# Kernel tuning notes

Measured on AMD Instinct MI355X. Metric: run time of the kernel, lower is better.

Reference implementation:

```python
import jax, jax.numpy as jnp
import numpy as np

B, S, H, NH, L, NS = 8, 4096, 768, 12, 2, 64
DH = H // NH
EPS = 1e-12


def _layer_norm(x, g, b):
    mu = jnp.mean(x, axis=-1, keepdims=True)
    var = jnp.mean((x - mu) ** 2, axis=-1, keepdims=True)
    return (x - mu) / jnp.sqrt(var + EPS) * g + b


def setup_inputs() -> dict:
    key = jax.random.key(0)
    ks = jax.random.split(key, 8)
    # sentence index per token: 64 equal contiguous sentences; position 0 is [CLS] in sentence 0
    sent_ind = jnp.broadcast_to((jnp.arange(S, dtype=jnp.int32) * NS) // S, (B, S)).astype(jnp.int32)
    start_layer = jax.random.normal(ks[0], (B, S, H), dtype=jnp.float32)
    init = lambda k, shape: (jax.random.normal(k, shape, dtype=jnp.float32) * 0.02)
    return {
        "sent_ind": sent_ind,
        "start_layer": start_layer,
        "Wq": init(ks[1], (L, H, H)), "bq": jnp.zeros((L, H), jnp.float32),
        "Wk": init(ks[2], (L, H, H)), "bk": jnp.zeros((L, H), jnp.float32),
        "Wv": init(ks[3], (L, H, H)), "bv": jnp.zeros((L, H), jnp.float32),
        "Wo": init(ks[4], (L, H, H)), "bo": jnp.zeros((L, H), jnp.float32),
        "ln_g": jnp.ones((L, H), jnp.float32), "ln_b": jnp.zeros((L, H), jnp.float32),
    }


def reference(sent_ind, start_layer, Wq, bq, Wk, bk, Wv, bv, Wo, bo, ln_g, ln_b):
    # ---- segment-mean pooling by sentence index (vectorized replacement of the python loops) ----
    onehot = (sent_ind[..., None] == jnp.arange(NS, dtype=sent_ind.dtype)).astype(start_layer.dtype)  # [B,S,NS]
    # the first [CLS] token is excluded from sentence 0's mean
    onehot = onehot.at[:, 0, :].set(0.0)
    sums = jnp.einsum('bsn,bsd->bnd', onehot, start_layer)          # [B,NS,H]
    counts = jnp.sum(onehot, axis=1)                                 # [B,NS]
    x = sums / counts[..., None]                                     # graph_vectors [B,NS,H]

    # ---- GAT layers: BertSelfAttention + GATSelfOutput(dense->gelu->LayerNorm), dropout=eval ----
    scale = 1.0 / (DH ** 0.5)
    for i in range(L):
        q = (x @ Wq[i] + bq[i]).reshape(B, NS, NH, DH)
        k = (x @ Wk[i] + bk[i]).reshape(B, NS, NH, DH)
        v = (x @ Wv[i] + bv[i]).reshape(B, NS, NH, DH)
        scores = jnp.einsum('bqhd,bkhd->bhqk', q, k) * scale
        probs = jax.nn.softmax(scores, axis=-1)
        ctx = jnp.einsum('bhqk,bkhd->bqhd', probs, v).reshape(B, NS, H)
        h = jax.nn.gelu(ctx @ Wo[i] + bo[i], approximate=False)
        x = _layer_norm(h, ln_g[i], ln_b[i])
    return x
```

## Files before the change

### kernel.cpp

```cpp
#include <hip/hip_runtime.h>
#include <hip/hip_bf16.h>

constexpr int cB  = 8;
constexpr int cS  = 4096;
constexpr int cH  = 768;
constexpr int cNH = 12;
constexpr int cL  = 2;
constexpr int cNS = 64;
constexpr int cDH = 64;
constexpr int cM  = cB * cNS;

typedef __attribute__((ext_vector_type(8))) short bf16x8;
typedef __attribute__((ext_vector_type(4))) float f32x4;

union PrepShared {
    float T[64][65];
    struct { int cnt; int list[cS]; } p;
};

__global__ __launch_bounds__(256) void prep_kernel(
    const int* __restrict__ sent_ind, const float* __restrict__ sl,
    __hip_bfloat16* __restrict__ xb,
    const float* __restrict__ Wq, const float* __restrict__ Wk,
    const float* __restrict__ Wv, const float* __restrict__ Wo,
    __hip_bfloat16* __restrict__ wt)
{
    __shared__ PrepShared sh;
    int tid = threadIdx.x;

    if (blockIdx.x < (unsigned)cM) {
        int bn = blockIdx.x;
        int b = bn >> 6, n = bn & (cNS - 1);
        if (tid == 0) sh.p.cnt = 0;
        __syncthreads();
        const int* si = sent_ind + (size_t)b * cS;
        for (int s = tid; s < cS; s += 256)
            if (s != 0 && si[s] == n) { int p = atomicAdd(&sh.p.cnt, 1); sh.p.list[p] = s; }
        __syncthreads();
        int c = sh.p.cnt;
        if (tid < 192) {
            const float* bbase = sl + (size_t)b * cS * cH;
            int col = tid * 4;
            float4 a0 = {0.f, 0.f, 0.f, 0.f};
            float4 a1 = {0.f, 0.f, 0.f, 0.f};
            float4 a2 = {0.f, 0.f, 0.f, 0.f};
            float4 a3 = {0.f, 0.f, 0.f, 0.f};
            int i = 0;
            for (; i + 4 <= c; i += 4) {
                float4 r0 = *(const float4*)(bbase + (size_t)sh.p.list[i + 0] * cH + col);
                float4 r1 = *(const float4*)(bbase + (size_t)sh.p.list[i + 1] * cH + col);
                float4 r2 = *(const float4*)(bbase + (size_t)sh.p.list[i + 2] * cH + col);
                float4 r3 = *(const float4*)(bbase + (size_t)sh.p.list[i + 3] * cH + col);
                a0.x += r0.x; a0.y += r0.y; a0.z += r0.z; a0.w += r0.w;
                a1.x += r1.x; a1.y += r1.y; a1.z += r1.z; a1.w += r1.w;
                a2.x += r2.x; a2.y += r2.y; a2.z += r2.z; a2.w += r2.w;
                a3.x += r3.x; a3.y += r3.y; a3.z += r3.z; a3.w += r3.w;
            }
            for (; i < c; ++i) {
                float4 r0 = *(const float4*)(bbase + (size_t)sh.p.list[i] * cH + col);
                a0.x += r0.x; a0.y += r0.y; a0.z += r0.z; a0.w += r0.w;
            }
            float inv = 1.0f / (float)c;
            __hip_bfloat16* xr = xb + (size_t)bn * cH + col;
            xr[0] = __float2bfloat16((a0.x + a1.x + a2.x + a3.x) * inv);
            xr[1] = __float2bfloat16((a0.y + a1.y + a2.y + a3.y) * inv);
            xr[2] = __float2bfloat16((a0.z + a1.z + a2.z + a3.z) * inv);
            xr[3] = __float2bfloat16((a0.w + a1.w + a2.w + a3.w) * inv);
        }
    } else {
        int bi = blockIdx.x - cM;
        int bx = bi % 12, by = (bi / 12) % 12, mat = bi / 144;
        int layer = mat >> 2, which = mat & 3;
        const float* W = (which == 0 ? Wq : which == 1 ? Wk : which == 2 ? Wv : Wo)
                         + (size_t)layer * cH * cH;
        int k0 = by * 64, n0 = bx * 64;
        int r = tid >> 2, cb = (tid & 3) * 16;
        #pragma unroll
        for (int u = 0; u < 4; ++u) {
            float4 w4 = *(const float4*)(W + (size_t)(k0 + r) * cH + n0 + cb + u * 4);
            sh.T[r][cb + u * 4 + 0] = w4.x; sh.T[r][cb + u * 4 + 1] = w4.y;
            sh.T[r][cb + u * 4 + 2] = w4.z; sh.T[r][cb + u * 4 + 3] = w4.w;
        }
        __syncthreads();
        int kk = tid & 63;
        int nb = (tid >> 6) * 16;
        __hip_bfloat16* dst = wt + ((size_t)mat * cH + n0) * cH + k0;
        #pragma unroll
        for (int u = 0; u < 16; ++u) {
            int nn = nb + u;
            dst[(size_t)nn * cH + kk] = __float2bfloat16(sh.T[kk][nn]);
        }
    }
}

struct AttnShared {
    float QP[cNS][cDH + 4];
    float Ks[cNS][cDH + 4];
    float Vt[cDH][cNS + 4];
};

__global__ __launch_bounds__(256) void qkvattn_kernel(
    const __hip_bfloat16* __restrict__ x_bf,
    const __hip_bfloat16* __restrict__ wqkv,
    const float* __restrict__ bq, const float* __restrict__ bk,
    const float* __restrict__ bv,
    __hip_bfloat16* __restrict__ ctx_bf)
{
    __shared__ AttnShared sh;
    int tid = threadIdx.x;
    int lane = tid & 63, wave = tid >> 6;
    int l15 = lane & 15, q4 = lane >> 4;
    int b = blockIdx.x / cNH, hh = blockIdx.x % cNH;

    const __hip_bfloat16* Arow[4];
    #pragma unroll
    for (int m = 0; m < 4; ++m)
        Arow[m] = x_bf + (size_t)(b * 64 + m * 16 + l15) * cH + q4 * 8;
    const __hip_bfloat16* Brow[3];
    int cmat[3], cnt_[3];
    #pragma unroll
    for (int j = 0; j < 3; ++j) {
        int c = wave * 3 + j;
        cmat[j] = c >> 2; cnt_[j] = c & 3;
        Brow[j] = wqkv + (size_t)cmat[j] * cH * cH
                       + (size_t)(hh * 64 + cnt_[j] * 16 + l15) * cH + q4 * 8;
    }

    f32x4 acc[3][4];
    #pragma unroll
    for (int j = 0; j < 3; ++j)
        #pragma unroll
        for (int m = 0; m < 4; ++m) acc[j][m] = (f32x4){0.f, 0.f, 0.f, 0.f};

    #pragma unroll 4
    for (int k0 = 0; k0 < cH; k0 += 32) {
        bf16x8 a[4], bb8[3];
        #pragma unroll
        for (int m = 0; m < 4; ++m) a[m] = *(const bf16x8*)(Arow[m] + k0);
        #pragma unroll
        for (int j = 0; j < 3; ++j) bb8[j] = *(const bf16x8*)(Brow[j] + k0);
        #pragma unroll
        for (int j = 0; j < 3; ++j)
            #pragma unroll
            for (int m = 0; m < 4; ++m)
                acc[j][m] = __builtin_amdgcn_mfma_f32_16x16x32_bf16(a[m], bb8[j], acc[j][m], 0, 0, 0);
    }

    const float scale = 0.125f;
    #pragma unroll
    for (int j = 0; j < 3; ++j) {
        int mat = cmat[j], nt = cnt_[j];
        int col_d = nt * 16 + l15;
        int col_g = hh * 64 + col_d;
        float bias = (mat == 0 ? bq : mat == 1 ? bk : bv)[col_g];
        #pragma unroll
        for (int m = 0; m < 4; ++m) {
            #pragma unroll
            for (int r = 0; r < 4; ++r) {
                int row_s = m * 16 + q4 * 4 + r;
                float v = acc[j][m][r] + bias;
                if (mat == 0)      sh.QP[row_s][col_d] = v * scale;
                else if (mat == 1) sh.Ks[row_s][col_d] = v;
                else               sh.Vt[col_d][row_s] = v;
            }
        }
    }
    __syncthreads();

    int tx = tid & 15, ty = tid >> 4;
    float accs[4][4] = {};
    for (int d = 0; d < cDH; d += 4) {
        float4 qv[4], kv[4];
        #pragma unroll
        for (int i = 0; i < 4; ++i) qv[i] = *(const float4*)&sh.QP[ty * 4 + i][d];
        #pragma unroll
        for (int j = 0; j < 4; ++j) kv[j] = *(const float4*)&sh.Ks[tx + j * 16][d];
        #pragma unroll
        for (int i = 0; i < 4; ++i)
            #pragma unroll
            for (int j = 0; j < 4; ++j)
                accs[i][j] += qv[i].x * kv[j].x + qv[i].y * kv[j].y +
                              qv[i].z * kv[j].z + qv[i].w * kv[j].w;
    }
    __syncthreads();
    #pragma unroll
    for (int i = 0; i < 4; ++i)
        #pragma unroll
        for (int j = 0; j < 4; ++j)
            sh.QP[ty * 4 + i][tx + j * 16] = accs[i][j];
    __syncthreads();

    {
        int row = tid >> 2, jq = tid & 3;
        float e[16];
        float m = -1e30f;
        #pragma unroll
        for (int c = 0; c < 16; ++c) { e[c] = sh.QP[row][jq * 16 + c]; m = fmaxf(m, e[c]); }
        m = fmaxf(m, __shfl_xor(m, 1));
        m = fmaxf(m, __shfl_xor(m, 2));
        float s = 0.f;
        #pragma unroll
        for (int c = 0; c < 16; ++c) { e[c] = __expf(e[c] - m); s += e[c]; }
        s += __shfl_xor(s, 1);
        s += __shfl_xor(s, 2);
        float inv = 1.0f / s;
        #pragma unroll
        for (int c = 0; c < 16; ++c) sh.QP[row][jq * 16 + c] = e[c] * inv;
    }
    __syncthreads();

    float acco[4][4] = {};
    for (int c = 0; c < cNS; c += 4) {
        float4 p4[4], vt4[4];
        #pragma unroll
        for (int i = 0; i < 4; ++i) p4[i] = *(const float4*)&sh.QP[ty * 4 + i][c];
        #pragma unroll
        for (int j = 0; j < 4; ++j) vt4[j] = *(const float4*)&sh.Vt[tx + j * 16][c];
        #pragma unroll
        for (int i = 0; i < 4; ++i)
            #pragma unroll
            for (int j = 0; j < 4; ++j)
                acco[i][j] += p4[i].x * vt4[j].x + p4[i].y * vt4[j].y +
                              p4[i].z * vt4[j].z + p4[i].w * vt4[j].w;
    }
    size_t base = ((size_t)b * cNS) * cH + hh * cDH;
    #pragma unroll
    for (int i = 0; i < 4; ++i)
        #pragma unroll
        for (int j = 0; j < 4; ++j)
            ctx_bf[base + (size_t)(ty * 4 + i) * cH + tx + j * 16] =
                __float2bfloat16(acco[i][j]);
}

__global__ __launch_bounds__(256) void oln_kernel(
    const __hip_bfloat16* __restrict__ ctx_bf,
    const __hip_bfloat16* __restrict__ wto,
    const float* __restrict__ bo,
    const float* __restrict__ g, const float* __restrict__ bb,
    __hip_bfloat16* __restrict__ xb, float* __restrict__ outf)
{
    __shared__ float part[4][16][2];
    int tid = threadIdx.x;
    int lane = tid & 63, wave = tid >> 6;
    int l15 = lane & 15, q4 = lane >> 4;
    int r0 = blockIdx.x * 16;

    const __hip_bfloat16* Arow = ctx_bf + (size_t)(r0 + l15) * cH + q4 * 8;
    const __hip_bfloat16* Brow[12];
    #pragma unroll
    for (int nt = 0; nt < 12; ++nt)
        Brow[nt] = wto + (size_t)(wave * 192 + nt * 16 + l15) * cH + q4 * 8;

    f32x4 acc[12];
    #pragma unroll
    for (int nt = 0; nt < 12; ++nt) acc[nt] = (f32x4){0.f, 0.f, 0.f, 0.f};

    #pragma unroll 2
    for (int k0 = 0; k0 < cH; k0 += 32) {
        bf16x8 a = *(const bf16x8*)(Arow + k0);
        #pragma unroll
        for (int nt = 0; nt < 12; ++nt) {
            bf16x8 b8 = *(const bf16x8*)(Brow[nt] + k0);
            acc[nt] = __builtin_amdgcn_mfma_f32_16x16x32_bf16(a, b8, acc[nt], 0, 0, 0);
        }
    }

    float rs[4] = {0.f, 0.f, 0.f, 0.f}, rq[4] = {0.f, 0.f, 0.f, 0.f};
    #pragma unroll
    for (int nt = 0; nt < 12; ++nt) {
        int col = wave * 192 + nt * 16 + l15;
        float bv = bo[col];
        #pragma unroll
        for (int r = 0; r < 4; ++r) {
            float v = acc[nt][r] + bv;
            v = 0.5f * v * (1.0f + erff(v * 0.70710678118654752f));
            acc[nt][r] = v;
            rs[r] += v;
            rq[r] += v * v;
        }
    }
    #pragma unroll
    for (int o = 8; o; o >>= 1) {
        #pragma unroll
        for (int r = 0; r < 4; ++r) {
            rs[r] += __shfl_xor(rs[r], o);
            rq[r] += __shfl_xor(rq[r], o);
        }
    }
    if (l15 == 0) {
        #pragma unroll
        for (int r = 0; r < 4; ++r) {
            part[wave][q4 * 4 + r][0] = rs[r];
            part[wave][q4 * 4 + r][1] = rq[r];
        }
    }
    __syncthreads();
    #pragma unroll
    for (int r = 0; r < 4; ++r) {
        int row = q4 * 4 + r;
        float S  = part[0][row][0] + part[1][row][0] + part[2][row][0] + part[3][row][0];
        float Q2 = part[0][row][1] + part[1][row][1] + part[2][row][1] + part[3][row][1];
        float mu  = S * (1.0f / 768.0f);
        float var = Q2 * (1.0f / 768.0f) - mu * mu;
        float inv = rsqrtf(var + 1e-12f);
        int row_g = r0 + row;
        #pragma unroll
        for (int nt = 0; nt < 12; ++nt) {
            int col = wave * 192 + nt * 16 + l15;
            float o = (acc[nt][r] - mu) * inv * g[col] + bb[col];
            xb[(size_t)row_g * cH + col] = __float2bfloat16(o);
            if (outf) outf[(size_t)row_g * cH + col] = o;
        }
    }
}

extern "C" void kernel_launch(void* const* d_in, const int* in_sizes, int n_in,
                              void* d_out, int out_size, void* d_ws, size_t ws_size,
                              hipStream_t stream) {
    const int*   sent_ind = (const int*)d_in[0];
    const float* start    = (const float*)d_in[1];
    const float* Wq = (const float*)d_in[2];
    const float* bq = (const float*)d_in[3];
    const float* Wk = (const float*)d_in[4];
    const float* bk = (const float*)d_in[5];
    const float* Wv = (const float*)d_in[6];
    const float* bv = (const float*)d_in[7];
    const float* Wo = (const float*)d_in[8];
    const float* bo = (const float*)d_in[9];
    const float* ln_g = (const float*)d_in[10];
    const float* ln_b = (const float*)d_in[11];
    float* out = (float*)d_out;

    char* w = (char*)d_ws;
    __hip_bfloat16* wt     = (__hip_bfloat16*)w;
    __hip_bfloat16* x_bf   = (__hip_bfloat16*)(w + 9437184);
    __hip_bfloat16* ctx_bf = (__hip_bfloat16*)(w + 9437184 + 786432);

    prep_kernel<<<cM + 1152, 256, 0, stream>>>(sent_ind, start, x_bf,
                                               Wq, Wk, Wv, Wo, wt);

    for (int i = 0; i < cL; ++i) {
        const __hip_bfloat16* wqkv = wt + (size_t)(i * 4) * cH * cH;
        const __hip_bfloat16* wto  = wt + (size_t)(i * 4 + 3) * cH * cH;
        qkvattn_kernel<<<cB * cNH, 256, 0, stream>>>(
            x_bf, wqkv, bq + (size_t)i * cH, bk + (size_t)i * cH, bv + (size_t)i * cH,
            ctx_bf);
        oln_kernel<<<cM / 16, 256, 0, stream>>>(
            ctx_bf, wto, bo + (size_t)i * cH,
            ln_g + (size_t)i * cH, ln_b + (size_t)i * cH,
            x_bf, (i == cL - 1) ? out : nullptr);
    }
}
```

Before: 350.3 us.

## Split fused output GEMM+LayerNorm into wider-grid GEMM and separate LN kernel

```diff
diff --git a/kernel.cpp b/kernel.cpp
--- a/kernel.cpp
+++ b/kernel.cpp
@@ -232,85 +232,83 @@
                 __float2bfloat16(acco[i][j]);
 }
 
-__global__ __launch_bounds__(256) void oln_kernel(
-    const __hip_bfloat16* __restrict__ ctx_bf,
-    const __hip_bfloat16* __restrict__ wto,
-    const float* __restrict__ bo,
-    const float* __restrict__ g, const float* __restrict__ bb,
-    __hip_bfloat16* __restrict__ xb, float* __restrict__ outf)
+__global__ __launch_bounds__(256) void ogemm_kernel(
+    const __hip_bfloat16* __restrict__ A,
+    const __hip_bfloat16* __restrict__ Wt,
+    const float* __restrict__ bias,
+    __hip_bfloat16* __restrict__ C)
 {
-    __shared__ float part[4][16][2];
+    int lane = threadIdx.x & 63;
+    int wave = threadIdx.x >> 6;
+    int l15 = lane & 15, q4 = lane >> 4;
+    int m0 = blockIdx.y * 64 + wave * 16;
+    int n0 = blockIdx.x * 32;
+
+    const __hip_bfloat16* Arow = A  + (size_t)(m0 + l15) * cH + q4 * 8;
+    const __hip_bfloat16* Wr0  = Wt + (size_t)(n0 + l15) * cH + q4 * 8;
+    const __hip_bfloat16* Wr1  = Wr0 + (size_t)16 * cH;
+
+    f32x4 acc0 = {0.f, 0.f, 0.f, 0.f};
+    f32x4 acc1 = {0.f, 0.f, 0.f, 0.f};
+    #pragma unroll 8
+    for (int k0 = 0; k0 < cH; k0 += 32) {
+        bf16x8 a  = *(const bf16x8*)(Arow + k0);
+        bf16x8 b0 = *(const bf16x8*)(Wr0 + k0);
+        bf16x8 b1 = *(const bf16x8*)(Wr1 + k0);
+        acc0 = __builtin_amdgcn_mfma_f32_16x16x32_bf16(a, b0, acc0, 0, 0, 0);
+        acc1 = __builtin_amdgcn_mfma_f32_16x16x32_bf16(a, b1, acc1, 0, 0, 0);
+    }
+    #pragma unroll
+    for (int nt = 0; nt < 2; ++nt) {
+        const f32x4 acc = nt == 0 ? acc0 : acc1;
+        int col = n0 + nt * 16 + l15;
+        float bv = bias[col];
+        #pragma unroll
+        for (int r = 0; r < 4; ++r) {
+            float v = acc[r] + bv;
+            v = 0.5f * v * (1.0f + erff(v * 0.70710678118654752f));
+            C[(size_t)(m0 + q4 * 4 + r) * cH + col] = __float2bfloat16(v);
+        }
+    }
+}
+
+__global__ __launch_bounds__(256) void ln_kernel(
+    const __hip_bfloat16* __restrict__ h, const float* __restrict__ g,
+    const float* __restrict__ bb, __hip_bfloat16* __restrict__ xb,
+    float* __restrict__ outf)
+{
+    int row = blockIdx.x;
+    const __hip_bfloat16* r = h + (size_t)row * cH;
     int tid = threadIdx.x;
-    int lane = tid & 63, wave = tid >> 6;
-    int l15 = lane & 15, q4 = lane >> 4;
-    int r0 = blockIdx.x * 16;
-
-    const __hip_bfloat16* Arow = ctx_bf + (size_t)(r0 + l15) * cH + q4 * 8;
-    const __hip_bfloat16* Brow[12];
-    #pragma unroll
-    for (int nt = 0; nt < 12; ++nt)
-        Brow[nt] = wto + (size_t)(wave * 192 + nt * 16 + l15) * cH + q4 * 8;
-
-    f32x4 acc[12];
-    #pragma unroll
-    for (int nt = 0; nt < 12; ++nt) acc[nt] = (f32x4){0.f, 0.f, 0.f, 0.f};
-
-    #pragma unroll 2
-    for (int k0 = 0; k0 < cH; k0 += 32) {
-        bf16x8 a = *(const bf16x8*)(Arow + k0);
-        #pragma unroll
-        for (int nt = 0; nt < 12; ++nt) {
-            bf16x8 b8 = *(const bf16x8*)(Brow[nt] + k0);
-            acc[nt] = __builtin_amdgcn_mfma_f32_16x16x32_bf16(a, b8, acc[nt], 0, 0, 0);
-        }
-    }
-
-    float rs[4] = {0.f, 0.f, 0.f, 0.f}, rq[4] = {0.f, 0.f, 0.f, 0.f};
-    #pragma unroll
-    for (int nt = 0; nt < 12; ++nt) {
-        int col = wave * 192 + nt * 16 + l15;
-        float bv = bo[col];
-        #pragma unroll
-        for (int r = 0; r < 4; ++r) {
-            float v = acc[nt][r] + bv;
-            v = 0.5f * v * (1.0f + erff(v * 0.70710678118654752f));
-            acc[nt][r] = v;
-            rs[r] += v;
-            rq[r] += v * v;
-        }
-    }
-    #pragma unroll
-    for (int o = 8; o; o >>= 1) {
-        #pragma unroll
-        for (int r = 0; r < 4; ++r) {
-            rs[r] += __shfl_xor(rs[r], o);
-            rq[r] += __shfl_xor(rq[r], o);
-        }
-    }
-    if (l15 == 0) {
-        #pragma unroll
-        for (int r = 0; r < 4; ++r) {
-            part[wave][q4 * 4 + r][0] = rs[r];
-            part[wave][q4 * 4 + r][1] = rq[r];
-        }
-    }
-    __syncthreads();
-    #pragma unroll
-    for (int r = 0; r < 4; ++r) {
-        int row = q4 * 4 + r;
-        float S  = part[0][row][0] + part[1][row][0] + part[2][row][0] + part[3][row][0];
-        float Q2 = part[0][row][1] + part[1][row][1] + part[2][row][1] + part[3][row][1];
-        float mu  = S * (1.0f / 768.0f);
-        float var = Q2 * (1.0f / 768.0f) - mu * mu;
-        float inv = rsqrtf(var + 1e-12f);
-        int row_g = r0 + row;
-        #pragma unroll
-        for (int nt = 0; nt < 12; ++nt) {
-            int col = wave * 192 + nt * 16 + l15;
-            float o = (acc[nt][r] - mu) * inv * g[col] + bb[col];
-            xb[(size_t)row_g * cH + col] = __float2bfloat16(o);
-            if (outf) outf[(size_t)row_g * cH + col] = o;
-        }
+    float v0 = __bfloat162float(r[tid]);
+    float v1 = __bfloat162float(r[tid + 256]);
+    float v2 = __bfloat162float(r[tid + 512]);
+    float s = v0 + v1 + v2;
+    __shared__ float red[4];
+    #pragma unroll
+    for (int o = 32; o; o >>= 1) s += __shfl_xor(s, o);
+    if ((tid & 63) == 0) red[tid >> 6] = s;
+    __syncthreads();
+    float mu = (red[0] + red[1] + red[2] + red[3]) * (1.0f / 768.0f);
+    float d0 = v0 - mu, d1 = v1 - mu, d2 = v2 - mu;
+    float ss = d0 * d0 + d1 * d1 + d2 * d2;
+    __syncthreads();
+    #pragma unroll
+    for (int o = 32; o; o >>= 1) ss += __shfl_xor(ss, o);
+    if ((tid & 63) == 0) red[tid >> 6] = ss;
+    __syncthreads();
+    float var = (red[0] + red[1] + red[2] + red[3]) * (1.0f / 768.0f);
+    float inv = rsqrtf(var + 1e-12f);
+    float o0 = d0 * inv * g[tid]       + bb[tid];
+    float o1 = d1 * inv * g[tid + 256] + bb[tid + 256];
+    float o2 = d2 * inv * g[tid + 512] + bb[tid + 512];
+    __hip_bfloat16* xr = xb + (size_t)row * cH;
+    xr[tid]       = __float2bfloat16(o0);
+    xr[tid + 256] = __float2bfloat16(o1);
+    xr[tid + 512] = __float2bfloat16(o2);
+    if (outf) {
+        float* orow = outf + (size_t)row * cH;
+        orow[tid] = o0; orow[tid + 256] = o1; orow[tid + 512] = o2;
     }
 }
 
@@ -335,6 +333,7 @@
     __hip_bfloat16* wt     = (__hip_bfloat16*)w;
     __hip_bfloat16* x_bf   = (__hip_bfloat16*)(w + 9437184);
     __hip_bfloat16* ctx_bf = (__hip_bfloat16*)(w + 9437184 + 786432);
+    __hip_bfloat16* hb     = (__hip_bfloat16*)(w + 9437184 + 2 * 786432);
 
     prep_kernel<<<cM + 1152, 256, 0, stream>>>(sent_ind, start, x_bf,
                                                Wq, Wk, Wv, Wo, wt);
@@ -345,9 +344,10 @@
         qkvattn_kernel<<<cB * cNH, 256, 0, stream>>>(
             x_bf, wqkv, bq + (size_t)i * cH, bk + (size_t)i * cH, bv + (size_t)i * cH,
             ctx_bf);
-        oln_kernel<<<cM / 16, 256, 0, stream>>>(
-            ctx_bf, wto, bo + (size_t)i * cH,
-            ln_g + (size_t)i * cH, ln_b + (size_t)i * cH,
+        ogemm_kernel<<<dim3(24, 8), 256, 0, stream>>>(
+            ctx_bf, wto, bo + (size_t)i * cH, hb);
+        ln_kernel<<<cM, 256, 0, stream>>>(
+            hb, ln_g + (size_t)i * cH, ln_b + (size_t)i * cH,
             x_bf, (i == cL - 1) ? out : nullptr);
     }
 }
```

Result: faster. 287.2 us (-18.0%).
